# Kernel optimization log

Hardware: AMD Instinct MI355X
Metric: run time of the kernel (lower is better)

Reference implementation:

```python
import jax, jax.numpy as jnp
import numpy as np

NUM_CLASSES = 1000
TEMPERATURE = 0.1
B, B_OOD, D = 4096, 4096, 512


def _l2norm(x):
    return x / jnp.linalg.norm(x, axis=-1, keepdims=True)


def setup_inputs() -> dict:
    key = jax.random.key(0)
    k1, k2, k3, k4, k5 = jax.random.split(key, 5)
    return {
        "centers1": _l2norm(jax.random.normal(k1, (NUM_CLASSES, D), dtype=jnp.float32)),
        "features": _l2norm(jax.random.normal(k2, (B, D), dtype=jnp.float32)),
        "targets": jax.random.randint(k3, (B,), 0, NUM_CLASSES, dtype=jnp.int64 if jax.config.jax_enable_x64 else jnp.int32),
        "features_ood": _l2norm(jax.random.normal(k4, (B_OOD, D), dtype=jnp.float32)),
        "pseudo_target_ood": jax.random.randint(k5, (B_OOD,), 0, NUM_CLASSES, dtype=jnp.int64 if jax.config.jax_enable_x64 else jnp.int32),
    }


def reference(centers1, features, targets, features_ood, pseudo_target_ood):
    C = centers1.shape[0]
    b = features.shape[0]
    bo = features_ood.shape[0]
    n = b + C + bo  # total anchors: batch + class centers + ood

    centers_lbl = jnp.arange(C, dtype=targets.dtype)
    ood_lbl = jnp.full((bo,), C, dtype=targets.dtype)  # ood gets label == num_classes
    targets_all = jnp.concatenate([targets, centers_lbl, ood_lbl])              # [N]
    targets_all_class = jnp.concatenate([targets, centers_lbl, pseudo_target_ood])  # [N]

    # per-class count over all N labels (pseudo labels for ood)
    batch_cls_count = jnp.zeros((C,), dtype=jnp.float32).at[targets_all_class].add(1.0)

    # positive mask: same label as anchor, excluding self (diagonal for j < B)
    mask = (targets_all[:b, None] == targets_all[None, :]).astype(jnp.float32)  # [B,N]
    logits_mask = 1.0 - (jnp.arange(n)[None, :] == jnp.arange(b)[:, None]).astype(jnp.float32)
    mask = mask * logits_mask

    features_all = jnp.concatenate([features, centers1, features_ood], axis=0)  # [N,D]
    logits = jnp.matmul(features, features_all.T) / TEMPERATURE                 # [B,N]
    logits = logits - jax.lax.stop_gradient(jnp.max(logits, axis=1, keepdims=True))

    exp_logits = jnp.exp(logits) * logits_mask
    # class-balanced per-instance weight (count of the column's class, minus positive mask)
    per_ins_weight = batch_cls_count[targets_all_class][None, :] - mask         # [B,N]
    exp_logits_sum = jnp.sum(exp_logits / per_ins_weight, axis=1, keepdims=True)
    log_prob = logits - jnp.log(exp_logits_sum)

    mean_log_prob_pos = jnp.sum(mask * log_prob, axis=1) / jnp.sum(mask, axis=1)
    loss = -jnp.mean(mean_log_prob_pos)
    return loss
```

## Files before the change

kernel.cpp:

```cpp
#include <hip/hip_runtime.h>
#include <stdint.h>

#define NUM_C 1000
#define NB    4096
#define NCOL  9192
#define NPAD  9216
#define DK    512
#define BM    128
#define BN    256
#define BKB   32
#define INV_T 10.0f

typedef __attribute__((ext_vector_type(4))) float f32x4;

#define OFF_FALL  0u
#define OFF_CNTP  4718592u
#define OFF_CNTTP 4784128u
#define OFF_S     4849664u
#define OFF_P     4866048u

__device__ __forceinline__ void async16(const void* g, void* l) {
  __builtin_amdgcn_global_load_lds((const __attribute__((address_space(1))) void*)g,
                                   (__attribute__((address_space(3))) void*)l,
                                   16, 0, 0);
}

__device__ __forceinline__ unsigned sw_e4m3(float x) {
  float ax = fabsf(x);
  unsigned s = (__float_as_uint(x) >> 24) & 0x80u;
  if (ax < 0.015625f) {
    int n = (int)rintf(ax * 512.0f);
    if (n >= 8) return s | 0x08u;
    return s | (unsigned)n;
  }
  if (ax >= 448.0f) return s | 0x7Eu;
  unsigned u = __float_as_uint(ax);
  int ee = (int)(u >> 23) - 127;
  float scale = __uint_as_float((unsigned)(3 - ee + 127) << 23);
  int qv = (int)rintf(ax * scale);
  if (qv == 16) { ee++; qv = 8; }
  return s | (unsigned)(((ee + 7) << 3) | (qv - 8));
}

template <bool HI>
__device__ __forceinline__ int cvt2(float a, float b, int old) {
#if __has_builtin(__builtin_amdgcn_cvt_pk_fp8_f32)
  return __builtin_amdgcn_cvt_pk_fp8_f32(a, b, old, HI);
#else
  unsigned pk = sw_e4m3(a) | (sw_e4m3(b) << 8);
  return HI ? (int)(((unsigned)old & 0x0000FFFFu) | (pk << 16))
            : (int)(((unsigned)old & 0xFFFF0000u) | pk);
#endif
}

__global__ __launch_bounds__(256) void prep_k(const float* __restrict__ centers,
                                              const float* __restrict__ feats,
                                              const float* __restrict__ ood,
                                              const int* __restrict__ targets,
                                              const int* __restrict__ pseudo,
                                              unsigned char* __restrict__ fall,
                                              unsigned* __restrict__ cntP,
                                              unsigned* __restrict__ cntTP,
                                              float* __restrict__ SP) {
  __shared__ unsigned hc[1024];
  __shared__ unsigned hct[1024];
  const int tid = threadIdx.x;

  int idx = blockIdx.x * 256 + tid;
  int row = idx >> 5;
  int ck  = (idx & 31) * 16;
  const float* src = nullptr;
  if (row < NB)              src = feats   + (size_t)row * DK + ck;
  else if (row < NB + NUM_C) src = centers + (size_t)(row - NB) * DK + ck;
  else if (row < NCOL)       src = ood     + (size_t)(row - NB - NUM_C) * DK + ck;
  unsigned w[4] = {0u, 0u, 0u, 0u};
  if (src) {
#pragma unroll
    for (int g = 0; g < 4; g++) {
      float4 v0 = *(const float4*)(src + g * 4);
      int p = 0;
      p = cvt2<false>(v0.x, v0.y, p);
      p = cvt2<true>(v0.z, v0.w, p);
      w[g] = (unsigned)p;
    }
  }
  *(uint4*)(fall + (size_t)row * DK + ck) = make_uint4(w[0], w[1], w[2], w[3]);

  if (blockIdx.x < 16) {
    for (int k = tid; k < 1024; k += 256) { hc[k] = 0u; hct[k] = 0u; }
    __syncthreads();
    int i = blockIdx.x * 256 + tid;
    int t = targets[i];
    atomicAdd(&hc[t], 1u);
    atomicAdd(&hct[t], 1u);
    atomicAdd(&hc[pseudo[i]], 1u);
    __syncthreads();
    for (int k = tid; k < 1024; k += 256) {
      cntP[blockIdx.x * 1024 + k]  = hc[k];
      cntTP[blockIdx.x * 1024 + k] = hct[k];
    }
  } else if (blockIdx.x < 48) {
    SP[(blockIdx.x - 16) * 256 + tid] = 0.0f;
  }
}

__global__ __launch_bounds__(256, 2) void gemm_fused(const unsigned char* __restrict__ fall,
                                                     const int* __restrict__ targets,
                                                     const int* __restrict__ pseudo,
                                                     const unsigned* __restrict__ cntP,
                                                     float* __restrict__ Sacc,
                                                     float* __restrict__ Pacc) {
  __shared__ unsigned char As[2][BM * BKB];
  __shared__ unsigned char Bs[2][BN * BKB];
  __shared__ int    sLbl[BN];
  __shared__ float  sRw0[BN];
  __shared__ float  sRw1[BN];
  __shared__ int    sTgt[BM];

  const int tid   = threadIdx.x;
  const int nTile = blockIdx.x;
  const int mTile = blockIdx.y;
  const int lane  = tid & 63;
  const int wv    = tid >> 6;
  const int wm    = wv >> 1;
  const int wn    = wv & 1;
  const int q     = lane >> 4;
  const int cIdx  = lane & 15;

  const int aRow0 = mTile * BM;
  const int bRow0 = nTile * BN;

  const int sRow = tid >> 1;
  const int cg   = (tid & 1) ^ (sRow & 1);
  const unsigned char* gA  = fall + (size_t)(aRow0 + sRow)       * DK + cg * 16;
  const unsigned char* gB0 = fall + (size_t)(bRow0 + sRow)       * DK + cg * 16;
  const unsigned char* gB1 = fall + (size_t)(bRow0 + 128 + sRow) * DK + cg * 16;
  const int lOff = tid * 16;

  async16(gA,        &As[0][lOff]);
  async16(gB0,       &Bs[0][lOff]);
  async16(gB1,       &Bs[0][lOff + 4096]);

  {
    int j = nTile * BN + tid;
    int lbl, tac;
    if (j >= NCOL)         { lbl = -1; tac = -1; }
    else if (j < NB)       { tac = targets[j]; lbl = tac; }
    else if (j < NB+NUM_C) { tac = j - NB;     lbl = tac; }
    else                   { tac = pseudo[j - NB - NUM_C]; lbl = NUM_C; }
    sLbl[tid] = lbl;
    if (tac >= 0) {
      unsigned c = 1u;
#pragma unroll
      for (int b = 0; b < 16; b++) c += cntP[b * 1024 + tac];
      float w = (float)c;
      sRw0[tid] = 1.0f / w;
      sRw1[tid] = 1.0f / (w - 1.0f);
    } else {
      sRw0[tid] = 0.f;
      sRw1[tid] = 0.f;
    }
    if (tid < BM) sTgt[tid] = targets[mTile * BM + tid];
  }

  f32x4 acc[4][8];
#pragma unroll
  for (int mi = 0; mi < 4; mi++)
#pragma unroll
    for (int ni = 0; ni < 8; ni++)
      acc[mi][ni] = (f32x4){0.f, 0.f, 0.f, 0.f};

  const int fOff = ((((q >> 1) ^ (cIdx & 1)) << 4) | ((q & 1) << 3));

  __syncthreads();

#pragma unroll
  for (int it = 0; it < 16; it++) {
    const int cur = it & 1;
    const int nxt = cur ^ 1;
    if (it < 15) {
      const int kt = (it + 1) * BKB;
      async16(gA + kt,  &As[nxt][lOff]);
      async16(gB0 + kt, &Bs[nxt][lOff]);
      async16(gB1 + kt, &Bs[nxt][lOff + 4096]);
    }

    long long af[4];
    long long bf8[8];
#pragma unroll
    for (int mi = 0; mi < 4; mi++)
      af[mi] = *(const long long*)&As[cur][(wm * 64 + mi * 16 + cIdx) * BKB + fOff];
#pragma unroll
    for (int ni = 0; ni < 8; ni++)
      bf8[ni] = *(const long long*)&Bs[cur][(wn * 128 + ni * 16 + cIdx) * BKB + fOff];
#pragma unroll
    for (int mi = 0; mi < 4; mi++)
#pragma unroll
      for (int ni = 0; ni < 8; ni++)
        acc[mi][ni] = __builtin_amdgcn_mfma_f32_16x16x32_fp8_fp8(af[mi], bf8[ni], acc[mi][ni], 0, 0, 0);

    __syncthreads();
  }

  float vS[16], vP[16];
#pragma unroll
  for (int s = 0; s < 16; s++) { vS[s] = 0.f; vP[s] = 0.f; }

#pragma unroll
  for (int ni = 0; ni < 8; ni++) {
    int jloc = wn * 128 + ni * 16 + cIdx;
    int j    = nTile * BN + jloc;
    int lblj = sLbl[jloc];
    float rw0 = sRw0[jloc], rw1 = sRw1[jloc];
#pragma unroll
    for (int mi = 0; mi < 4; mi++) {
      f32x4 a = acc[mi][ni];
#pragma unroll
      for (int r = 0; r < 4; r++) {
        int iloc = wm * 64 + mi * 16 + q * 4 + r;
        int i    = mTile * BM + iloc;
        int ti   = sTgt[iloc];
        float l  = a[r] * INV_T;
        bool diag = (j == i);
        bool pos  = (lblj == ti) && !diag;
        float rw  = diag ? 0.0f : (pos ? rw1 : rw0);
        float e   = __expf(l - 10.0f) * rw;
        vS[mi * 4 + r] += e;
        vP[mi * 4 + r] += pos ? l : 0.0f;
      }
    }
  }

#define RED_STEP(m, s, h)                                        \
  {                                                              \
    float sendS = (cIdx & (m)) ? vS[(s)] : vS[(s) + (h)];        \
    float sendP = (cIdx & (m)) ? vP[(s)] : vP[(s) + (h)];        \
    float rS = __shfl_xor(sendS, (m), 64);                       \
    float rP = __shfl_xor(sendP, (m), 64);                       \
    vS[(s)] = ((cIdx & (m)) ? vS[(s) + (h)] : vS[(s)]) + rS;     \
    vP[(s)] = ((cIdx & (m)) ? vP[(s) + (h)] : vP[(s)]) + rP;     \
  }
  RED_STEP(8, 0, 8) RED_STEP(8, 1, 8) RED_STEP(8, 2, 8) RED_STEP(8, 3, 8)
  RED_STEP(8, 4, 8) RED_STEP(8, 5, 8) RED_STEP(8, 6, 8) RED_STEP(8, 7, 8)
  RED_STEP(4, 0, 4) RED_STEP(4, 1, 4) RED_STEP(4, 2, 4) RED_STEP(4, 3, 4)
  RED_STEP(2, 0, 2) RED_STEP(2, 1, 2)
  RED_STEP(1, 0, 1)
#undef RED_STEP

  {
    int rowLoc = wm * 64 + (cIdx >> 2) * 16 + q * 4 + (cIdx & 3);
    int i = mTile * BM + rowLoc;
    atomicAdd(&Sacc[i], vS[0]);
    atomicAdd(&Pacc[i], vP[0]);
  }
}

__global__ __launch_bounds__(256) void finalize_k(const float* __restrict__ S,
                                                  const float* __restrict__ P,
                                                  const int* __restrict__ targets,
                                                  const unsigned* __restrict__ cntTP,
                                                  float* __restrict__ out) {
  __shared__ unsigned ct[1024];
  __shared__ float red[4];
  int tid = threadIdx.x;
  for (int k = tid; k < 1024; k += 256) {
    unsigned c = 0u;
#pragma unroll
    for (int b = 0; b < 16; b++) c += cntTP[b * 1024 + k];
    ct[k] = c;
  }
  __syncthreads();
  float local = 0.f;
  for (int i = tid; i < NB; i += 256) {
    float npos = (float)ct[targets[i]];
    local += P[i] / npos - INV_T - __logf(S[i]);
  }
  for (int m = 1; m < 64; m <<= 1) local += __shfl_xor(local, m, 64);
  if ((tid & 63) == 0) red[tid >> 6] = local;
  __syncthreads();
  if (tid == 0) {
    float t = red[0] + red[1] + red[2] + red[3];
    out[0] = -t / (float)NB;
  }
}

extern "C" void kernel_launch(void* const* d_in, const int* in_sizes, int n_in,
                              void* d_out, int out_size, void* d_ws, size_t ws_size,
                              hipStream_t stream) {
  const float* centers = (const float*)d_in[0];
  const float* feats   = (const float*)d_in[1];
  const int*   targets = (const int*)d_in[2];
  const float* ood     = (const float*)d_in[3];
  const int*   pseudo  = (const int*)d_in[4];

  char* ws = (char*)d_ws;
  unsigned char* fall  = (unsigned char*)(ws + OFF_FALL);
  unsigned*      cntP  = (unsigned*)(ws + OFF_CNTP);
  unsigned*      cntTP = (unsigned*)(ws + OFF_CNTTP);
  float*         Sacc  = (float*)(ws + OFF_S);
  float*         Pacc  = (float*)(ws + OFF_P);

  prep_k<<<dim3((NPAD * 32) / 256), 256, 0, stream>>>(centers, feats, ood, targets, pseudo,
                                                      fall, cntP, cntTP, Sacc);
  gemm_fused<<<dim3(NPAD / BN, NB / BM), 256, 0, stream>>>(fall, targets, pseudo, cntP, Sacc, Pacc);
  finalize_k<<<1, 256, 0, stream>>>(Sacc, Pacc, targets, cntTP, (float*)d_out);
}
```

Baseline: 139.1 us.

## Fold finalize into GEMM via last-block-done counter; transpose count histograms

After: 203.3 us. +46.1%, slower.

```diff
diff --git a/kernel.cpp b/kernel.cpp
--- a/kernel.cpp
+++ b/kernel.cpp
@@ -10,6 +10,7 @@
 #define BN    256
 #define BKB   32
 #define INV_T 10.0f
+#define NBLK  (36 * 32)
 
 typedef __attribute__((ext_vector_type(4))) float f32x4;
 
@@ -18,6 +19,7 @@
 #define OFF_CNTTP 4784128u
 #define OFF_S     4849664u
 #define OFF_P     4866048u
+#define OFF_DONE  4882432u
 
 __device__ __forceinline__ void async16(const void* g, void* l) {
   __builtin_amdgcn_global_load_lds((const __attribute__((address_space(1))) void*)g,
@@ -61,7 +63,7 @@
                                               unsigned char* __restrict__ fall,
                                               unsigned* __restrict__ cntP,
                                               unsigned* __restrict__ cntTP,
-                                              float* __restrict__ SP) {
+                                              unsigned* __restrict__ SPD) {
   __shared__ unsigned hc[1024];
   __shared__ unsigned hct[1024];
   const int tid = threadIdx.x;
@@ -96,11 +98,12 @@
     atomicAdd(&hc[pseudo[i]], 1u);
     __syncthreads();
     for (int k = tid; k < 1024; k += 256) {
-      cntP[blockIdx.x * 1024 + k]  = hc[k];
-      cntTP[blockIdx.x * 1024 + k] = hct[k];
-    }
-  } else if (blockIdx.x < 48) {
-    SP[(blockIdx.x - 16) * 256 + tid] = 0.0f;
+      cntP[k * 16 + blockIdx.x]  = hc[k];
+      cntTP[k * 16 + blockIdx.x] = hct[k];
+    }
+  } else if (blockIdx.x < 49) {
+    int i = (blockIdx.x - 16) * 256 + tid;
+    if (i < 8193) SPD[i] = 0u;
   }
 }
 
@@ -108,14 +111,19 @@
                                                      const int* __restrict__ targets,
                                                      const int* __restrict__ pseudo,
                                                      const unsigned* __restrict__ cntP,
+                                                     const unsigned* __restrict__ cntTP,
                                                      float* __restrict__ Sacc,
-                                                     float* __restrict__ Pacc) {
+                                                     float* __restrict__ Pacc,
+                                                     unsigned* __restrict__ done,
+                                                     float* __restrict__ out) {
   __shared__ unsigned char As[2][BM * BKB];
   __shared__ unsigned char Bs[2][BN * BKB];
   __shared__ int    sLbl[BN];
   __shared__ float  sRw0[BN];
   __shared__ float  sRw1[BN];
   __shared__ int    sTgt[BM];
+  __shared__ int    sLast;
+  __shared__ float  red[4];
 
   const int tid   = threadIdx.x;
   const int nTile = blockIdx.x;
@@ -150,9 +158,10 @@
     else                   { tac = pseudo[j - NB - NUM_C]; lbl = NUM_C; }
     sLbl[tid] = lbl;
     if (tac >= 0) {
-      unsigned c = 1u;
-#pragma unroll
-      for (int b = 0; b < 16; b++) c += cntP[b * 1024 + tac];
+      const uint4* p4 = (const uint4*)(cntP + tac * 16);
+      uint4 a0 = p4[0], a1 = p4[1], a2 = p4[2], a3 = p4[3];
+      unsigned c = 1u + a0.x + a0.y + a0.z + a0.w + a1.x + a1.y + a1.z + a1.w
+                      + a2.x + a2.y + a2.z + a2.w + a3.x + a3.y + a3.z + a3.w;
       float w = (float)c;
       sRw0[tid] = 1.0f / w;
       sRw1[tid] = 1.0f / (w - 1.0f);
@@ -253,34 +262,33 @@
     atomicAdd(&Sacc[i], vS[0]);
     atomicAdd(&Pacc[i], vP[0]);
   }
-}
-
-__global__ __launch_bounds__(256) void finalize_k(const float* __restrict__ S,
-                                                  const float* __restrict__ P,
-                                                  const int* __restrict__ targets,
-                                                  const unsigned* __restrict__ cntTP,
-                                                  float* __restrict__ out) {
-  __shared__ unsigned ct[1024];
-  __shared__ float red[4];
-  int tid = threadIdx.x;
-  for (int k = tid; k < 1024; k += 256) {
-    unsigned c = 0u;
-#pragma unroll
-    for (int b = 0; b < 16; b++) c += cntTP[b * 1024 + k];
-    ct[k] = c;
+
+  __threadfence();
+  if (tid == 0) {
+    unsigned old = atomicAdd(done, 1u);
+    sLast = (old == NBLK - 1) ? 1 : 0;
   }
   __syncthreads();
-  float local = 0.f;
-  for (int i = tid; i < NB; i += 256) {
-    float npos = (float)ct[targets[i]];
-    local += P[i] / npos - INV_T - __logf(S[i]);
-  }
-  for (int m = 1; m < 64; m <<= 1) local += __shfl_xor(local, m, 64);
-  if ((tid & 63) == 0) red[tid >> 6] = local;
-  __syncthreads();
-  if (tid == 0) {
-    float t = red[0] + red[1] + red[2] + red[3];
-    out[0] = -t / (float)NB;
+  if (sLast) {
+    __threadfence();
+    float local = 0.f;
+    for (int i = tid; i < NB; i += 256) {
+      float S  = __hip_atomic_load(&Sacc[i], __ATOMIC_RELAXED, __HIP_MEMORY_SCOPE_AGENT);
+      float Pv = __hip_atomic_load(&Pacc[i], __ATOMIC_RELAXED, __HIP_MEMORY_SCOPE_AGENT);
+      int t = targets[i];
+      const uint4* p4 = (const uint4*)(cntTP + t * 16);
+      uint4 a0 = p4[0], a1 = p4[1], a2 = p4[2], a3 = p4[3];
+      unsigned c = a0.x + a0.y + a0.z + a0.w + a1.x + a1.y + a1.z + a1.w
+                 + a2.x + a2.y + a2.z + a2.w + a3.x + a3.y + a3.z + a3.w;
+      local += Pv / (float)c - INV_T - __logf(S);
+    }
+    for (int m = 1; m < 64; m <<= 1) local += __shfl_xor(local, m, 64);
+    if ((tid & 63) == 0) red[tid >> 6] = local;
+    __syncthreads();
+    if (tid == 0) {
+      float t = red[0] + red[1] + red[2] + red[3];
+      out[0] = -t / (float)NB;
+    }
   }
 }
 
@@ -299,9 +307,10 @@
   unsigned*      cntTP = (unsigned*)(ws + OFF_CNTTP);
   float*         Sacc  = (float*)(ws + OFF_S);
   float*         Pacc  = (float*)(ws + OFF_P);
+  unsigned*      done  = (unsigned*)(ws + OFF_DONE);
 
   prep_k<<<dim3((NPAD * 32) / 256), 256, 0, stream>>>(centers, feats, ood, targets, pseudo,
-                                                      fall, cntP, cntTP, Sacc);
-  gemm_fused<<<dim3(NPAD / BN, NB / BM), 256, 0, stream>>>(fall, targets, pseudo, cntP, Sacc, Pacc);
-  finalize_k<<<1, 256, 0, stream>>>(Sacc, Pacc, targets, cntTP, (float*)d_out);
-}
+                                                      fall, cntP, cntTP, (unsigned*)(ws + OFF_S));
+  gemm_fused<<<dim3(NPAD / BN, NB / BM), 256, 0, stream>>>(fall, targets, pseudo, cntP, cntTP,
+                                                           Sacc, Pacc, done, (float*)d_out);
+}
```
